# Kernel optimization log

Measured on AMD Instinct MI355X. Metric: run time of the kernel, lower is better.

Reference implementation:

```python
import jax, jax.numpy as jnp
import numpy as np

B, N, F_IN, F_OUT = 64, 1024, 200, 200
NEG_SLOPE = 0.2  # PyG GATConv default


def setup_inputs() -> dict:
    key = jax.random.key(0)
    k1, k2, k3, k4, k5 = jax.random.split(key, 5)
    return {
        "x": jax.random.normal(k1, (B, 1, N, F_IN), dtype=jnp.float32),
        "W": jax.random.normal(k2, (F_IN, F_OUT), dtype=jnp.float32) * 0.05,
        "att_src": jax.random.normal(k3, (F_OUT,), dtype=jnp.float32) * 0.05,
        "att_dst": jax.random.normal(k4, (F_OUT,), dtype=jnp.float32) * 0.05,
        "bias": jax.random.normal(k5, (F_OUT,), dtype=jnp.float32) * 0.05,
    }


def reference(x, W, att_src, att_dst, bias):
    # x: [B, 1, N, F_IN]; module flattens to (B*N) nodes but the edge_index
    # only spans node ids 0..N-1 (complete graph minus self loops). PyG's
    # GATConv re-adds self loops for ALL B*N nodes, so:
    #   nodes 0..N-1 : dense softmax attention over all N nodes (incl. self)
    #   nodes >= N   : only the self loop -> out = h_i + bias
    b, _, n, f = x.shape
    xf = x.reshape(b * n, f)
    h = xf @ W                                # [B*N, F_OUT] linear transform

    h0 = h[:n]                                # first graph's nodes
    a_s = h0 @ att_src                        # [N] per-source score
    a_d = h0 @ att_dst                        # [N] per-target score
    # score[i, j] = leaky_relu(a_dst[i] + a_src[j]), softmax over sources j
    scores = jax.nn.leaky_relu(a_d[:, None] + a_s[None, :], negative_slope=NEG_SLOPE)
    alpha = jax.nn.softmax(scores, axis=1)    # [N, N]
    out0 = alpha @ h0 + bias                  # [N, F_OUT]

    out_rest = h[n:] + bias                   # self-loop only -> alpha == 1
    out = jnp.concatenate([out0, out_rest], axis=0)
    return out.reshape(b, n, -1)[:, None]     # [B, 1, N, F_OUT]
```

## Files before the change

### kernel.cpp

```cpp
#include <hip/hip_runtime.h>

#define BATCH 64
#define NNODE 1024
#define FDIM  200
#define MROWS (BATCH * NNODE)
#define NEG_SLOPE 0.2f

#define NKT 7
#define NNT 13
#define KTBYTES (NNT * 1024)

typedef short s16x8 __attribute__((ext_vector_type(8)));
typedef float f32x4 __attribute__((ext_vector_type(4)));


__device__ __forceinline__ unsigned int f2bf(float f) {
    unsigned int u = __float_as_uint(f);
    return (u + 0x7fffu + ((u >> 16) & 1u)) >> 16;
}
__device__ __forceinline__ unsigned int pack2(float a, float b) {
    return f2bf(a) | (f2bf(b) << 16);
}

__global__ __launch_bounds__(64) void k_prep(const float* __restrict__ W,
                                             const float* __restrict__ att_src,
                                             const float* __restrict__ att_dst,
                                             unsigned short* __restrict__ fragW,
                                             float* __restrict__ wsv,
                                             float* __restrict__ wdv)
{
    const int b    = blockIdx.x;
    const int lane = threadIdx.x;

    if (b < 91) {
        const int kt   = b / NNT;
        const int nt   = b - kt * NNT;
        const int n    = nt * 16 + (lane & 15);
        const int kb   = kt * 32 + (lane >> 4) * 8;
        s16x8 v;
        #pragma unroll
        for (int j = 0; j < 8; ++j) {
            int k = kb + j;
            float f = (k < FDIM && n < FDIM) ? W[k * FDIM + n] : 0.f;
            v[j] = (short)f2bf(f);
        }
        ((s16x8*)(fragW + (size_t)b * 512))[lane] = v;
    } else {
        const int kk = b - 91;
        const float* Wr = W + kk * FDIM;
        float ps = 0.f, pd = 0.f;
        #pragma unroll
        for (int i = 0; i < 4; ++i) {
            int n = lane + i * 64;
            if (n < FDIM) {
                float wv = Wr[n];
                ps = fmaf(wv, att_src[n], ps);
                pd = fmaf(wv, att_dst[n], pd);
            }
        }
        #pragma unroll
        for (int off = 32; off; off >>= 1) {
            ps += __shfl_down(ps, off);
            pd += __shfl_down(pd, off);
        }
        if (lane == 0) { wsv[kk] = ps; wdv[kk] = pd; }
    }
}

__global__ __launch_bounds__(256) void k_av(const float* __restrict__ x,
                                            const float* __restrict__ wsv,
                                            const float* __restrict__ wdv,
                                            float* __restrict__ a_s,
                                            float* __restrict__ a_d)
{
    const int tid  = threadIdx.x;
    const int lane = tid & 63;
    const int row  = blockIdx.x * 4 + (tid >> 6);
    const float* xr = x + (size_t)row * FDIM;
    float ss = 0.f, sd = 0.f;
    for (int k = lane; k < FDIM; k += 64) {
        float xv = xr[k];
        ss = fmaf(xv, wsv[k], ss);
        sd = fmaf(xv, wdv[k], sd);
    }
    #pragma unroll
    for (int off = 32; off; off >>= 1) {
        ss += __shfl_down(ss, off);
        sd += __shfl_down(sd, off);
    }
    if (lane == 0) { a_s[row] = ss; a_d[row] = sd; }
}

__global__ __launch_bounds__(256, 4) void k_gemm(const float* __restrict__ x,
                                                 const unsigned short* __restrict__ fragW,
                                                 const float* __restrict__ bias,
                                                 float* __restrict__ out,
                                                 unsigned short* __restrict__ h0frag)
{
    __shared__ __align__(16) unsigned short Bs[2][2 * KTBYTES / 2];
    const int tid  = threadIdx.x;
    const int lane = tid & 63;
    const int w    = __builtin_amdgcn_readfirstlane(tid >> 6);
    const int ln   = lane & 15;
    const int quad = lane >> 4;
    const int R0   = blockIdx.x * 64;
    const int row0 = R0 + w * 16;

#define STAGE(kt0_, ntile_, buf_)                                             \
    {                                                                         \
        const char* gsrc = (const char*)fragW + (size_t)(kt0_) * KTBYTES;     \
        char* lbase = (char*)&Bs[buf_][0];                                    \
        const int ngroups = (ntile_) * NNT;                                   \
        _Pragma("unroll")                                                     \
        for (int i = 0; i < 7; ++i) {                                         \
            int g = i * 4 + w;                                                \
            if (g < ngroups)                                                  \
                __builtin_amdgcn_global_load_lds(                             \
                    (const __attribute__((address_space(1))) void*)           \
                        (gsrc + g * 1024 + lane * 16),                        \
                    (__attribute__((address_space(3))) void*)                 \
                        (lbase + g * 1024),                                   \
                    16, 0, 0);                                                \
        }                                                                     \
    }

#define LOADA(p_, slot_)                                                      \
    {                                                                         \
        const int kt0_ = 2 * (p_);                                            \
        if (kt0_ < 6) {                                                       \
            const float4* ap = (const float4*)(xrow + kt0_ * 32 + quad * 8);  \
            ar[slot_][0][0] = ap[0]; ar[slot_][0][1] = ap[1];                 \
        } else {                                                              \
            if (quad == 0) {                                                  \
                const float4* ap = (const float4*)(xrow + kt0_ * 32);         \
                ar[slot_][0][0] = ap[0]; ar[slot_][0][1] = ap[1];             \
            } else {                                                          \
                ar[slot_][0][0] = make_float4(0.f, 0.f, 0.f, 0.f);            \
                ar[slot_][0][1] = make_float4(0.f, 0.f, 0.f, 0.f);            \
            }                                                                 \
        }                                                                     \
        if (kt0_ + 1 < NKT) {                                                 \
            const float4* ap = (const float4*)(xrow + (kt0_ + 1) * 32 + quad * 8); \
            ar[slot_][1][0] = ap[0]; ar[slot_][1][1] = ap[1];                 \
        }                                                                     \
    }

    f32x4 acc[NNT];
    #pragma unroll
    for (int nt = 0; nt < NNT; ++nt) acc[nt] = (f32x4){0.f, 0.f, 0.f, 0.f};

    const float* xrow = x + (size_t)(row0 + ln) * FDIM;
    float4 ar[2][2][2];

    LOADA(0, 0);
    STAGE(0, 2, 0);
    __syncthreads();

    #pragma unroll
    for (int p = 0; p < 4; ++p) {
        const int cur = p & 1;
        if (p < 3) {
            STAGE(2 * (p + 1), ((p < 2) ? 2 : 1), cur ^ 1);
            LOADA(p + 1, cur ^ 1);
        }
        {
            float4 f0 = ar[cur][0][0], f1 = ar[cur][0][1];
            unsigned int au[4] = {pack2(f0.x, f0.y), pack2(f0.z, f0.w),
                                  pack2(f1.x, f1.y), pack2(f1.z, f1.w)};
            s16x8 a = *(s16x8*)au;
            const unsigned short* bbase = &Bs[cur][0];
            #pragma unroll
            for (int nt = 0; nt < NNT; ++nt) {
                s16x8 b = *(const s16x8*)(bbase + nt * 512 + lane * 8);
                acc[nt] = __builtin_amdgcn_mfma_f32_16x16x32_bf16(a, b, acc[nt], 0, 0, 0);
            }
        }
        if (p < 3) {
            float4 f0 = ar[cur][1][0], f1 = ar[cur][1][1];
            unsigned int au[4] = {pack2(f0.x, f0.y), pack2(f0.z, f0.w),
                                  pack2(f1.x, f1.y), pack2(f1.z, f1.w)};
            s16x8 a = *(s16x8*)au;
            const unsigned short* bbase = &Bs[cur][0] + (KTBYTES / 2);
            #pragma unroll
            for (int nt = 0; nt < NNT; ++nt) {
                s16x8 b = *(const s16x8*)(bbase + nt * 512 + lane * 8);
                acc[nt] = __builtin_amdgcn_mfma_f32_16x16x32_bf16(a, b, acc[nt], 0, 0, 0);
            }
        }
        __syncthreads();
    }
#undef STAGE
#undef LOADA

    if (R0 >= NNODE) {
        #pragma unroll
        for (int nt = 0; nt < NNT; ++nt) {
            int col = nt * 16 + ln;
            if (nt < 12 || ln < 8) {
                float bv = bias[col];
                #pragma unroll
                for (int r = 0; r < 4; ++r)
                    out[(size_t)(row0 + quad * 4 + r) * FDIM + col] = acc[nt][r] + bv;
            }
        }
    } else {
        float* scrw = (float*)&Bs[0][0] + w * (16 * 17);
        const int kt2 = row0 >> 5;
        const int lo  = (row0 >> 4) & 1;
        for (int nt = 0; nt < NNT; ++nt) {
            #pragma unroll
            for (int r = 0; r < 4; ++r) scrw[(quad * 4 + r) * 17 + ln] = acc[nt][r];
            __syncthreads();
            if (lane < 32) {
                int oct = lane >> 4, nl = lane & 15;
                uint4 dv;
                dv.x = pack2(scrw[(oct * 8 + 0) * 17 + nl], scrw[(oct * 8 + 1) * 17 + nl]);
                dv.y = pack2(scrw[(oct * 8 + 2) * 17 + nl], scrw[(oct * 8 + 3) * 17 + nl]);
                dv.z = pack2(scrw[(oct * 8 + 4) * 17 + nl], scrw[(oct * 8 + 5) * 17 + nl]);
                dv.w = pack2(scrw[(oct * 8 + 6) * 17 + nl], scrw[(oct * 8 + 7) * 17 + nl]);
                *(uint4*)(h0frag + ((size_t)(kt2 * NNT + nt) * 64 + lo * 32 + lane) * 8) = dv;
            }
            __syncthreads();
        }
    }
}

__global__ __launch_bounds__(256) void k_stats(const float* __restrict__ a_s,
                                               const float* __restrict__ a_d,
                                               float* __restrict__ m_out,
                                               float* __restrict__ l_out)
{
    __shared__ float as_s[1024];
    const int tid = threadIdx.x;
    #pragma unroll
    for (int i = 0; i < 4; ++i) as_s[tid + i * 256] = a_s[tid + i * 256];
    __syncthreads();

    const int lane = tid & 63;
    const int row  = blockIdx.x * 4 + (tid >> 6);

    float mx = -1e30f;
    #pragma unroll
    for (int i = 0; i < 16; ++i) mx = fmaxf(mx, as_s[lane + i * 64]);
    #pragma unroll
    for (int off = 32; off; off >>= 1) mx = fmaxf(mx, __shfl_down(mx, off));
    mx = __shfl(mx, 0);

    const float ad = a_d[row];
    float mi = ad + mx; mi = (mi > 0.f) ? mi : NEG_SLOPE * mi;

    float sum = 0.f;
    #pragma unroll
    for (int i = 0; i < 16; ++i) {
        float s = ad + as_s[lane + i * 64];
        s = (s > 0.f) ? s : NEG_SLOPE * s;
        sum += __expf(s - mi);
    }
    #pragma unroll
    for (int off = 32; off; off >>= 1) sum += __shfl_down(sum, off);
    if (lane == 0) { m_out[row] = sum, m_out[row] = mi, l_out[row] = sum; }
}

__global__ __launch_bounds__(256) void k_attn(const unsigned short* __restrict__ h0frag,
                                              const float* __restrict__ a_s,
                                              const float* __restrict__ a_d,
                                              const float* __restrict__ m_v,
                                              const float* __restrict__ l_v,
                                              const float* __restrict__ bias,
                                              float* __restrict__ out)
{
    __shared__ f32x4 red[3][64];
    const int tid  = threadIdx.x;
    const int lane = tid & 63;
    const int w    = __builtin_amdgcn_readfirstlane(tid >> 6);
    const int ln   = lane & 15;
    const int quad = lane >> 4;
    const int it   = blockIdx.x / NNT;
    const int nt   = blockIdx.x - it * NNT;
    const int i0   = it * 16;

    const float ad = a_d[i0 + ln];
    const float mi = m_v[i0 + ln];

    f32x4 accA = (f32x4){0.f, 0.f, 0.f, 0.f};
    f32x4 accB = (f32x4){0.f, 0.f, 0.f, 0.f};

    #pragma unroll
    for (int k8 = 0; k8 < 8; ++k8) {
        const int kt2 = w * 8 + k8;
        const float4* ap = (const float4*)(a_s + kt2 * 32 + quad * 8);
        float4 f0 = ap[0], f1 = ap[1];
        float e[8] = {f0.x, f0.y, f0.z, f0.w, f1.x, f1.y, f1.z, f1.w};
        #pragma unroll
        for (int j = 0; j < 8; ++j) {
            float s = ad + e[j];
            s = (s > 0.f) ? s : NEG_SLOPE * s;
            e[j] = __expf(s - mi);
        }
        unsigned int au[4] = {pack2(e[0], e[1]), pack2(e[2], e[3]),
                              pack2(e[4], e[5]), pack2(e[6], e[7])};
        s16x8 afrag = *(s16x8*)au;
        s16x8 b = *(const s16x8*)(h0frag + ((size_t)(kt2 * NNT + nt) * 64 + lane) * 8);
        if (k8 & 1) accB = __builtin_amdgcn_mfma_f32_16x16x32_bf16(afrag, b, accB, 0, 0, 0);
        else        accA = __builtin_amdgcn_mfma_f32_16x16x32_bf16(afrag, b, accA, 0, 0, 0);
    }

    f32x4 acc = accA + accB;
    if (w > 0) red[w - 1][lane] = acc;
    __syncthreads();

    if (w == 0) {
        #pragma unroll
        for (int ww = 0; ww < 3; ++ww) acc += red[ww][lane];
        const int col = nt * 16 + ln;
        if (nt < 12 || ln < 8) {
            float bv = bias[col];
            #pragma unroll
            for (int r = 0; r < 4; ++r) {
                float rl = 1.0f / l_v[i0 + quad * 4 + r];
                out[(size_t)(i0 + quad * 4 + r) * FDIM + col] = acc[r] * rl + bv;
            }
        }
    }
}

extern "C" void kernel_launch(void* const* d_in, const int* in_sizes, int n_in,
                              void* d_out, int out_size, void* d_ws, size_t ws_size,
                              hipStream_t stream)
{
    const float* x       = (const float*)d_in[0];
    const float* W       = (const float*)d_in[1];
    const float* att_src = (const float*)d_in[2];
    const float* att_dst = (const float*)d_in[3];
    const float* bias    = (const float*)d_in[4];
    float* out = (float*)d_out;
    char*  wsb = (char*)d_ws;

    unsigned short* h0frag = (unsigned short*)(wsb + 0);
    float* a_s   = (float*)(wsb + 425984);
    float* a_d   = (float*)(wsb + 430080);
    float* m_i   = (float*)(wsb + 434176);
    float* l_i   = (float*)(wsb + 438272);
    unsigned short* fragW = (unsigned short*)(wsb + 442368);
    float* wsv   = (float*)(wsb + 535552);
    float* wdv   = (float*)(wsb + 536352);

    k_prep <<<291,         64, 0, stream>>>(W, att_src, att_dst, fragW, wsv, wdv);
    k_av   <<<NNODE / 4,  256, 0, stream>>>(x, wsv, wdv, a_s, a_d);
    k_stats<<<NNODE / 4,  256, 0, stream>>>(a_s, a_d, m_i, l_i);
    k_gemm <<<MROWS / 64, 256, 0, stream>>>(x, fragW, bias, out, h0frag);
    k_attn <<<64 * NNT,   256, 0, stream>>>(h0frag, a_s, a_d, m_i, l_i, bias, out);
}
```

Baseline: 132.0 us.

## Fuse score projection into GEMM and softmax stats into attention kernel

Removes the k_av and k_stats launches. The first-graph GEMM blocks now compute a_s/a_d dot products from x, and each attention block recomputes the row max and sum over all 1024 sources in shared memory. The GEMM K-loop is also restructured to stage one k-tile per iteration, halving the LDS buffer, at the cost of more barriers. The aim is to cut launch overhead and global round-trips, while redundantly recomputing the softmax statistics in each of the 832 attention blocks.

```diff
diff --git a/kernel.cpp b/kernel.cpp
--- a/kernel.cpp
+++ b/kernel.cpp
@@ -20,6 +20,9 @@
 }
 __device__ __forceinline__ unsigned int pack2(float a, float b) {
     return f2bf(a) | (f2bf(b) << 16);
+}
+__device__ __forceinline__ float lrelu(float s) {
+    return (s > 0.f) ? s : NEG_SLOPE * s;
 }
 
 __global__ __launch_bounds__(64) void k_prep(const float* __restrict__ W,
@@ -67,37 +70,17 @@
     }
 }
 
-__global__ __launch_bounds__(256) void k_av(const float* __restrict__ x,
-                                            const float* __restrict__ wsv,
-                                            const float* __restrict__ wdv,
-                                            float* __restrict__ a_s,
-                                            float* __restrict__ a_d)
-{
-    const int tid  = threadIdx.x;
-    const int lane = tid & 63;
-    const int row  = blockIdx.x * 4 + (tid >> 6);
-    const float* xr = x + (size_t)row * FDIM;
-    float ss = 0.f, sd = 0.f;
-    for (int k = lane; k < FDIM; k += 64) {
-        float xv = xr[k];
-        ss = fmaf(xv, wsv[k], ss);
-        sd = fmaf(xv, wdv[k], sd);
-    }
-    #pragma unroll
-    for (int off = 32; off; off >>= 1) {
-        ss += __shfl_down(ss, off);
-        sd += __shfl_down(sd, off);
-    }
-    if (lane == 0) { a_s[row] = ss; a_d[row] = sd; }
-}
-
 __global__ __launch_bounds__(256, 4) void k_gemm(const float* __restrict__ x,
                                                  const unsigned short* __restrict__ fragW,
                                                  const float* __restrict__ bias,
+                                                 const float* __restrict__ wsv,
+                                                 const float* __restrict__ wdv,
                                                  float* __restrict__ out,
-                                                 unsigned short* __restrict__ h0frag)
+                                                 unsigned short* __restrict__ h0frag,
+                                                 float* __restrict__ a_s,
+                                                 float* __restrict__ a_d)
 {
-    __shared__ __align__(16) unsigned short Bs[2][2 * KTBYTES / 2];
+    __shared__ __align__(16) unsigned short Bs[2][KTBYTES / 2];
     const int tid  = threadIdx.x;
     const int lane = tid & 63;
     const int w    = __builtin_amdgcn_readfirstlane(tid >> 6);
@@ -106,15 +89,14 @@
     const int R0   = blockIdx.x * 64;
     const int row0 = R0 + w * 16;
 
-#define STAGE(kt0_, ntile_, buf_)                                             \
+#define STAGE(kt_, buf_)                                                      \
     {                                                                         \
-        const char* gsrc = (const char*)fragW + (size_t)(kt0_) * KTBYTES;     \
+        const char* gsrc = (const char*)fragW + (size_t)(kt_) * KTBYTES;      \
         char* lbase = (char*)&Bs[buf_][0];                                    \
-        const int ngroups = (ntile_) * NNT;                                   \
         _Pragma("unroll")                                                     \
-        for (int i = 0; i < 7; ++i) {                                         \
+        for (int i = 0; i < 4; ++i) {                                         \
             int g = i * 4 + w;                                                \
-            if (g < ngroups)                                                  \
+            if (g < NNT)                                                      \
                 __builtin_amdgcn_global_load_lds(                             \
                     (const __attribute__((address_space(1))) void*)           \
                         (gsrc + g * 1024 + lane * 16),                        \
@@ -126,23 +108,18 @@
 
 #define LOADA(p_, slot_)                                                      \
     {                                                                         \
-        const int kt0_ = 2 * (p_);                                            \
-        if (kt0_ < 6) {                                                       \
-            const float4* ap = (const float4*)(xrow + kt0_ * 32 + quad * 8);  \
-            ar[slot_][0][0] = ap[0]; ar[slot_][0][1] = ap[1];                 \
+        if ((p_) < 6) {                                                       \
+            const float4* ap = (const float4*)(xrow + (p_) * 32 + quad * 8);  \
+            ar[slot_][0] = ap[0]; ar[slot_][1] = ap[1];                       \
         } else {                                                              \
             if (quad == 0) {                                                  \
-                const float4* ap = (const float4*)(xrow + kt0_ * 32);         \
-                ar[slot_][0][0] = ap[0]; ar[slot_][0][1] = ap[1];             \
+                const float4* ap = (const float4*)(xrow + (p_) * 32);         \
+                ar[slot_][0] = ap[0]; ar[slot_][1] = ap[1];                   \
             } else {                                                          \
-                ar[slot_][0][0] = make_float4(0.f, 0.f, 0.f, 0.f);            \
-                ar[slot_][0][1] = make_float4(0.f, 0.f, 0.f, 0.f);            \
+                ar[slot_][0] = make_float4(0.f, 0.f, 0.f, 0.f);               \
+                ar[slot_][1] = make_float4(0.f, 0.f, 0.f, 0.f);               \
             }                                                                 \
         }                                                                     \
-        if (kt0_ + 1 < NKT) {                                                 \
-            const float4* ap = (const float4*)(xrow + (kt0_ + 1) * 32 + quad * 8); \
-            ar[slot_][1][0] = ap[0]; ar[slot_][1][1] = ap[1];                 \
-        }                                                                     \
     }
 
     f32x4 acc[NNT];
@@ -150,44 +127,30 @@
     for (int nt = 0; nt < NNT; ++nt) acc[nt] = (f32x4){0.f, 0.f, 0.f, 0.f};
 
     const float* xrow = x + (size_t)(row0 + ln) * FDIM;
-    float4 ar[2][2][2];
+    float4 ar[2][2];
 
     LOADA(0, 0);
-    STAGE(0, 2, 0);
+    STAGE(0, 0);
     __syncthreads();
 
     #pragma unroll
-    for (int p = 0; p < 4; ++p) {
-        const int cur = p & 1;
-        if (p < 3) {
-            STAGE(2 * (p + 1), ((p < 2) ? 2 : 1), cur ^ 1);
-            LOADA(p + 1, cur ^ 1);
-        }
-        {
-            float4 f0 = ar[cur][0][0], f1 = ar[cur][0][1];
-            unsigned int au[4] = {pack2(f0.x, f0.y), pack2(f0.z, f0.w),
-                                  pack2(f1.x, f1.y), pack2(f1.z, f1.w)};
-            s16x8 a = *(s16x8*)au;
-            const unsigned short* bbase = &Bs[cur][0];
-            #pragma unroll
-            for (int nt = 0; nt < NNT; ++nt) {
-                s16x8 b = *(const s16x8*)(bbase + nt * 512 + lane * 8);
-                acc[nt] = __builtin_amdgcn_mfma_f32_16x16x32_bf16(a, b, acc[nt], 0, 0, 0);
-            }
-        }
-        if (p < 3) {
-            float4 f0 = ar[cur][1][0], f1 = ar[cur][1][1];
-            unsigned int au[4] = {pack2(f0.x, f0.y), pack2(f0.z, f0.w),
-                                  pack2(f1.x, f1.y), pack2(f1.z, f1.w)};
-            s16x8 a = *(s16x8*)au;
-            const unsigned short* bbase = &Bs[cur][0] + (KTBYTES / 2);
-            #pragma unroll
-            for (int nt = 0; nt < NNT; ++nt) {
-                s16x8 b = *(const s16x8*)(bbase + nt * 512 + lane * 8);
-                acc[nt] = __builtin_amdgcn_mfma_f32_16x16x32_bf16(a, b, acc[nt], 0, 0, 0);
-            }
-        }
-        __syncthreads();
+    for (int kt = 0; kt < NKT; ++kt) {
+        const int cur = kt & 1;
+        if (kt < NKT - 1) {
+            STAGE(kt + 1, cur ^ 1);
+            LOADA(kt + 1, cur ^ 1);
+        }
+        float4 f0 = ar[cur][0], f1 = ar[cur][1];
+        unsigned int au[4] = {pack2(f0.x, f0.y), pack2(f0.z, f0.w),
+                              pack2(f1.x, f1.y), pack2(f1.z, f1.w)};
+        s16x8 a = *(s16x8*)au;
+        const unsigned short* bbase = &Bs[cur][0];
+        #pragma unroll
+        for (int nt = 0; nt < NNT; ++nt) {
+            s16x8 b = *(const s16x8*)(bbase + nt * 512 + lane * 8);
+            acc[nt] = __builtin_amdgcn_mfma_f32_16x16x32_bf16(a, b, acc[nt], 0, 0, 0);
+        }
+        if (kt < NKT - 1) __syncthreads();
     }
 #undef STAGE
 #undef LOADA
@@ -204,6 +167,30 @@
             }
         }
     } else {
+        {
+            float ps = 0.f, pd = 0.f;
+            #pragma unroll
+            for (int kt = 0; kt < NKT; ++kt) {
+                if (kt < 6 || quad == 0) {
+                    const float4* ap = (const float4*)(xrow + kt * 32 + quad * 8);
+                    float4 f0 = ap[0], f1 = ap[1];
+                    const float4* sp = (const float4*)(wsv + kt * 32 + quad * 8);
+                    const float4* dp = (const float4*)(wdv + kt * 32 + quad * 8);
+                    float4 s0 = sp[0], s1 = sp[1], d0 = dp[0], d1 = dp[1];
+                    ps += f0.x*s0.x + f0.y*s0.y + f0.z*s0.z + f0.w*s0.w
+                        + f1.x*s1.x + f1.y*s1.y + f1.z*s1.z + f1.w*s1.w;
+                    pd += f0.x*d0.x + f0.y*d0.y + f0.z*d0.z + f0.w*d0.w
+                        + f1.x*d1.x + f1.y*d1.y + f1.z*d1.z + f1.w*d1.w;
+                }
+            }
+            ps += __shfl_down(ps, 32); ps += __shfl_down(ps, 16);
+            pd += __shfl_down(pd, 32); pd += __shfl_down(pd, 16);
+            if (lane < 16) {
+                a_s[row0 + lane] = ps;
+                a_d[row0 + lane] = pd;
+            }
+        }
+        __syncthreads();
         float* scrw = (float*)&Bs[0][0] + w * (16 * 17);
         const int kt2 = row0 >> 5;
         const int lo  = (row0 >> 4) & 1;
@@ -225,50 +212,15 @@
     }
 }
 
-__global__ __launch_bounds__(256) void k_stats(const float* __restrict__ a_s,
-                                               const float* __restrict__ a_d,
-                                               float* __restrict__ m_out,
-                                               float* __restrict__ l_out)
-{
-    __shared__ float as_s[1024];
-    const int tid = threadIdx.x;
-    #pragma unroll
-    for (int i = 0; i < 4; ++i) as_s[tid + i * 256] = a_s[tid + i * 256];
-    __syncthreads();
-
-    const int lane = tid & 63;
-    const int row  = blockIdx.x * 4 + (tid >> 6);
-
-    float mx = -1e30f;
-    #pragma unroll
-    for (int i = 0; i < 16; ++i) mx = fmaxf(mx, as_s[lane + i * 64]);
-    #pragma unroll
-    for (int off = 32; off; off >>= 1) mx = fmaxf(mx, __shfl_down(mx, off));
-    mx = __shfl(mx, 0);
-
-    const float ad = a_d[row];
-    float mi = ad + mx; mi = (mi > 0.f) ? mi : NEG_SLOPE * mi;
-
-    float sum = 0.f;
-    #pragma unroll
-    for (int i = 0; i < 16; ++i) {
-        float s = ad + as_s[lane + i * 64];
-        s = (s > 0.f) ? s : NEG_SLOPE * s;
-        sum += __expf(s - mi);
-    }
-    #pragma unroll
-    for (int off = 32; off; off >>= 1) sum += __shfl_down(sum, off);
-    if (lane == 0) { m_out[row] = sum, m_out[row] = mi, l_out[row] = sum; }
-}
-
 __global__ __launch_bounds__(256) void k_attn(const unsigned short* __restrict__ h0frag,
                                               const float* __restrict__ a_s,
                                               const float* __restrict__ a_d,
-                                              const float* __restrict__ m_v,
-                                              const float* __restrict__ l_v,
                                               const float* __restrict__ bias,
                                               float* __restrict__ out)
 {
+    __shared__ __align__(16) float as_s[1024];
+    __shared__ float mls[16];
+    __shared__ float rls[16];
     __shared__ f32x4 red[3][64];
     const int tid  = threadIdx.x;
     const int lane = tid & 63;
@@ -279,8 +231,34 @@
     const int nt   = blockIdx.x - it * NNT;
     const int i0   = it * 16;
 
+    #pragma unroll
+    for (int i = 0; i < 4; ++i) as_s[tid + i * 256] = a_s[tid + i * 256];
+    __syncthreads();
+
+    float mx = -1e30f;
+    #pragma unroll
+    for (int i = 0; i < 16; ++i) mx = fmaxf(mx, as_s[lane + i * 64]);
+    #pragma unroll
+    for (int off = 32; off; off >>= 1) mx = fmaxf(mx, __shfl_down(mx, off));
+    mx = __shfl(mx, 0);
+
+    #pragma unroll
+    for (int rr = 0; rr < 4; ++rr) {
+        const int r  = w * 4 + rr;
+        const float adr = a_d[i0 + r];
+        const float mi  = lrelu(adr + mx);
+        float sum = 0.f;
+        #pragma unroll
+        for (int i = 0; i < 16; ++i)
+            sum += __expf(lrelu(adr + as_s[lane + i * 64]) - mi);
+        #pragma unroll
+        for (int off = 32; off; off >>= 1) sum += __shfl_down(sum, off);
+        if (lane == 0) { mls[r] = mi; rls[r] = 1.0f / sum; }
+    }
+    __syncthreads();
+
     const float ad = a_d[i0 + ln];
-    const float mi = m_v[i0 + ln];
+    const float mi = mls[ln];
 
     f32x4 accA = (f32x4){0.f, 0.f, 0.f, 0.f};
     f32x4 accB = (f32x4){0.f, 0.f, 0.f, 0.f};
@@ -288,15 +266,12 @@
     #pragma unroll
     for (int k8 = 0; k8 < 8; ++k8) {
         const int kt2 = w * 8 + k8;
-        const float4* ap = (const float4*)(a_s + kt2 * 32 + quad * 8);
+        const float4* ap = (const float4*)(as_s + kt2 * 32 + quad * 8);
         float4 f0 = ap[0], f1 = ap[1];
         float e[8] = {f0.x, f0.y, f0.z, f0.w, f1.x, f1.y, f1.z, f1.w};
         #pragma unroll
-        for (int j = 0; j < 8; ++j) {
-            float s = ad + e[j];
-            s = (s > 0.f) ? s : NEG_SLOPE * s;
-            e[j] = __expf(s - mi);
-        }
+        for (int j = 0; j < 8; ++j)
+            e[j] = __expf(lrelu(ad + e[j]) - mi);
         unsigned int au[4] = {pack2(e[0], e[1]), pack2(e[2], e[3]),
                               pack2(e[4], e[5]), pack2(e[6], e[7])};
         s16x8 afrag = *(s16x8*)au;
@@ -317,7 +292,7 @@
             float bv = bias[col];
             #pragma unroll
             for (int r = 0; r < 4; ++r) {
-                float rl = 1.0f / l_v[i0 + quad * 4 + r];
+                float rl = rls[quad * 4 + r];
                 out[(size_t)(i0 + quad * 4 + r) * FDIM + col] = acc[r] * rl + bv;
             }
         }
@@ -339,15 +314,11 @@
     unsigned short* h0frag = (unsigned short*)(wsb + 0);
     float* a_s   = (float*)(wsb + 425984);
     float* a_d   = (float*)(wsb + 430080);
-    float* m_i   = (float*)(wsb + 434176);
-    float* l_i   = (float*)(wsb + 438272);
     unsigned short* fragW = (unsigned short*)(wsb + 442368);
     float* wsv   = (float*)(wsb + 535552);
     float* wdv   = (float*)(wsb + 536352);
 
     k_prep <<<291,         64, 0, stream>>>(W, att_src, att_dst, fragW, wsv, wdv);
-    k_av   <<<NNODE / 4,  256, 0, stream>>>(x, wsv, wdv, a_s, a_d);
-    k_stats<<<NNODE / 4,  256, 0, stream>>>(a_s, a_d, m_i, l_i);
-    k_gemm <<<MROWS / 64, 256, 0, stream>>>(x, fragW, bias, out, h0frag);
-    k_attn <<<64 * NNT,   256, 0, stream>>>(h0frag, a_s, a_d, m_i, l_i, bias, out);
-}
+    k_gemm <<<MROWS / 64, 256, 0, stream>>>(x, fragW, bias, wsv, wdv, out, h0frag, a_s, a_d);
+    k_attn <<<64 * NNT,   256, 0, stream>>>(h0frag, a_s, a_d, bias, out);
+}
```

New measurement: 132.3 us. Within noise of the previous version (+0.2%).
